# Kernel tuning notes

Measured on AMD Instinct MI355X. Metric: run time of the kernel, lower is better.

## Reference

```python
import jax, jax.numpy as jnp
import numpy as np

DIM = 4096
N_HEADS = 32
N_KV_HEADS = 8
HEAD_DIM = 128
SEQ = 2048
REPEATS = N_HEADS // N_KV_HEADS
SCALE = HEAD_DIM ** -0.5


def setup_inputs() -> dict:
    key = jax.random.key(0)
    ks = jax.random.split(key, 7)
    x = jax.random.normal(ks[0], (SEQ, DIM), dtype=jnp.float32)
    # rotary freqs_cis = exp(i * pos * theta^(-2j/d)) -> cos/sin, shape (S, head_dim/2)
    theta = 10000.0
    inv_freq = 1.0 / (theta ** (np.arange(0, HEAD_DIM, 2, dtype=np.float32) / HEAD_DIM))
    ang = np.arange(SEQ, dtype=np.float32)[:, None] * inv_freq[None, :]
    freqs_cos = jnp.asarray(np.cos(ang), dtype=jnp.float32)
    freqs_sin = jnp.asarray(np.sin(ang), dtype=jnp.float32)
    s = 0.02
    wq = s * jax.random.normal(ks[1], (DIM, N_HEADS * HEAD_DIM), dtype=jnp.float32)
    wk = s * jax.random.normal(ks[2], (DIM, N_KV_HEADS * HEAD_DIM), dtype=jnp.float32)
    wv = s * jax.random.normal(ks[3], (DIM, N_KV_HEADS * HEAD_DIM), dtype=jnp.float32)
    wo = s * jax.random.normal(ks[4], (N_HEADS * HEAD_DIM, DIM), dtype=jnp.float32)
    return {"x": x, "freqs_cos": freqs_cos, "freqs_sin": freqs_sin,
            "wq": wq, "wk": wk, "wv": wv, "wo": wo}


def _rope(t, cos, sin):
    # t: (S, H, D); treat last dim as D/2 complex pairs and rotate by freqs_cis
    S, H, D = t.shape
    tr = t.reshape(S, H, D // 2, 2)
    t1, t2 = tr[..., 0], tr[..., 1]
    c = cos[:, None, :]  # (S, 1, D/2)
    s = sin[:, None, :]
    o1 = t1 * c - t2 * s
    o2 = t1 * s + t2 * c
    return jnp.stack([o1, o2], axis=-1).reshape(S, H, D)


def reference(x, freqs_cos, freqs_sin, wq, wk, wv, wo):
    S = x.shape[0]
    xq = (x @ wq).reshape(S, N_HEADS, HEAD_DIM)
    xk = (x @ wk).reshape(S, N_KV_HEADS, HEAD_DIM)
    xv = (x @ wv).reshape(S, N_KV_HEADS, HEAD_DIM)
    xq = _rope(xq, freqs_cos, freqs_sin)
    xk = _rope(xk, freqs_cos, freqs_sin)
    # cache=None path: key,val = xk,xv; repeat_kv via repeat_interleave on head dim
    key = jnp.repeat(xk, REPEATS, axis=1)  # (S, H, D)
    val = jnp.repeat(xv, REPEATS, axis=1)
    # scaled dot-product attention, mask=None (cache is None)
    scores = jnp.einsum('qhd,khd->hqk', xq, key) * SCALE  # (H, S, S)
    att = jax.nn.softmax(scores, axis=-1)
    out = jnp.einsum('hqk,khd->qhd', att, val)  # (S, H, D)
    out = out.reshape(S, N_HEADS * HEAD_DIM)
    return out @ wo
```

## Files before the change

kernel.cpp:

```cpp
#include <hip/hip_runtime.h>
#include <hip/hip_bf16.h>

#define SEQ   2048
#define DIM   4096
#define NH    32
#define NKV   8
#define HD    128
#define KVDIM 1024
#define SCALE 0.08838834764831845f

typedef __attribute__((ext_vector_type(8))) short bf16x8;
typedef __attribute__((ext_vector_type(4))) float f32x4;
typedef __attribute__((ext_vector_type(16))) float f32x16;

__device__ __forceinline__ ushort f2bf(float f) {
  __hip_bfloat16 h = __float2bfloat16(f);
  return *reinterpret_cast<ushort*>(&h);
}

typedef const __attribute__((address_space(1))) uint* gas_ptr;
typedef __attribute__((address_space(3))) uint* las_ptr;
__device__ __forceinline__ void async16(const ushort* g, ushort* l) {
  __builtin_amdgcn_global_load_lds((gas_ptr)g, (las_ptr)l, 16, 0, 0);
}

__device__ __forceinline__ uint cvtpk(float lo, float hi) {
  uint r;
  asm("v_cvt_pk_bf16_f32 %0, %1, %2" : "=v"(r) : "v"(lo), "v"(hi));
  return r;
}
__device__ __forceinline__ void plswap(uint& a, uint& b) {
  asm("v_permlane32_swap_b32 %0, %1" : "+v"(a), "+v"(b));
}

__global__ __launch_bounds__(256) void convert_f32_bf16(
    const float* __restrict__ in, ushort* __restrict__ out)
{
  int i = (blockIdx.x * 256 + threadIdx.x) * 8;
  float4 a = *(const float4*)(in + i);
  float4 b = *(const float4*)(in + i + 4);
  uint4 u;
  u.x = (uint)f2bf(a.x) | ((uint)f2bf(a.y) << 16);
  u.y = (uint)f2bf(a.z) | ((uint)f2bf(a.w) << 16);
  u.z = (uint)f2bf(b.x) | ((uint)f2bf(b.y) << 16);
  u.w = (uint)f2bf(b.z) | ((uint)f2bf(b.w) << 16);
  *(uint4*)(out + i) = u;
}

__global__ __launch_bounds__(256) void transpose_w(
    const float* __restrict__ W, ushort* __restrict__ WT, int K, int N)
{
  __shared__ float t[32][33];
  const int k0 = blockIdx.y * 32, n0 = blockIdx.x * 32;
  const int tid = threadIdx.x;
  {
    int r = tid >> 3, c0 = (tid & 7) * 4;
    float4 v = *(const float4*)(W + (size_t)(k0 + r) * N + n0 + c0);
    t[r][c0] = v.x; t[r][c0 + 1] = v.y; t[r][c0 + 2] = v.z; t[r][c0 + 3] = v.w;
  }
  __syncthreads();
  {
    int n = tid >> 3, kc = (tid & 7) * 4;
    ushort4 u;
    u.x = f2bf(t[kc + 0][n]); u.y = f2bf(t[kc + 1][n]);
    u.z = f2bf(t[kc + 2][n]); u.w = f2bf(t[kc + 3][n]);
    *(ushort4*)(WT + (size_t)(n0 + n) * K + k0 + kc) = u;
  }
}

__global__ __launch_bounds__(256) void gemm_bt(
    const ushort* __restrict__ A, const ushort* __restrict__ BT,
    void* __restrict__ Cv, void* __restrict__ C2v,
    int M, int N, int K, int mode)
{
  __shared__ __align__(16) ushort As[128 * 32];
  __shared__ __align__(16) ushort Bs[128 * 32];

  const int tid  = threadIdx.x;
  const int lane = tid & 63;
  const int w    = tid >> 6;
  const int wr = w >> 1, wc = w & 1;
  const int quad = lane >> 4, l16 = lane & 15;
  const int m0 = blockIdx.y * 128, n0 = blockIdx.x * 128;
  const int srow = lane >> 2;
  const int scol = (lane & 3) * 8;

  f32x4 acc[4][4];
#pragma unroll
  for (int bm = 0; bm < 4; ++bm)
#pragma unroll
    for (int bn = 0; bn < 4; ++bn)
      acc[bm][bn] = (f32x4){0.f, 0.f, 0.f, 0.f};

  for (int k0 = 0; k0 < K; k0 += 32) {
#pragma unroll
    for (int j = 0; j < 2; ++j) {
      const int rb = w * 32 + j * 16;
      async16(A  + (size_t)(m0 + rb + srow) * K + k0 + scol, &As[rb * 32]);
      async16(BT + (size_t)(n0 + rb + srow) * K + k0 + scol, &Bs[rb * 32]);
    }
    __syncthreads();

    bf16x8 af[4], bf[4];
#pragma unroll
    for (int bm = 0; bm < 4; ++bm)
      af[bm] = *(const bf16x8*)&As[(wr * 64 + bm * 16 + l16) * 32 + quad * 8];
#pragma unroll
    for (int bn = 0; bn < 4; ++bn)
      bf[bn] = *(const bf16x8*)&Bs[(wc * 64 + bn * 16 + l16) * 32 + quad * 8];
#pragma unroll
    for (int bm = 0; bm < 4; ++bm)
#pragma unroll
      for (int bn = 0; bn < 4; ++bn)
        acc[bm][bn] = __builtin_amdgcn_mfma_f32_16x16x32_bf16(
            af[bm], bf[bn], acc[bm][bn], 0, 0, 0);
    __syncthreads();
  }

  if (mode == 0) {
    ushort* C = (ushort*)Cv;
#pragma unroll
    for (int bm = 0; bm < 4; ++bm) {
      int rbase = m0 + wr * 64 + bm * 16 + quad * 4;
#pragma unroll
      for (int bn = 0; bn < 4; ++bn) {
        int col = n0 + wc * 64 + bn * 16 + l16;
#pragma unroll
        for (int i = 0; i < 4; ++i)
          C[(size_t)(rbase + i) * N + col] = f2bf(acc[bm][bn][i]);
      }
    }
  } else if (mode == 1) {
    float* C = (float*)Cv;
#pragma unroll
    for (int bm = 0; bm < 4; ++bm) {
      int rbase = m0 + wr * 64 + bm * 16 + quad * 4;
#pragma unroll
      for (int bn = 0; bn < 4; ++bn) {
        int col = n0 + wc * 64 + bn * 16 + l16;
#pragma unroll
        for (int i = 0; i < 4; ++i)
          C[(size_t)(rbase + i) * N + col] = acc[bm][bn][i];
      }
    }
  } else {
    if (n0 < 1024) {
      ushort* C = (ushort*)Cv;
#pragma unroll
      for (int bm = 0; bm < 4; ++bm) {
        int rbase = m0 + wr * 64 + bm * 16 + quad * 4;
#pragma unroll
        for (int bn = 0; bn < 4; ++bn) {
          int col = n0 + wc * 64 + bn * 16 + l16;
#pragma unroll
          for (int i = 0; i < 4; ++i)
            C[(size_t)(rbase + i) * KVDIM + col] = f2bf(acc[bm][bn][i]);
        }
      }
    } else {
      ushort* C2 = (ushort*)C2v;
#pragma unroll
      for (int bm = 0; bm < 4; ++bm) {
        int rbase = m0 + wr * 64 + bm * 16 + quad * 4;
#pragma unroll
        for (int bn = 0; bn < 4; ++bn) {
          int col = n0 + wc * 64 + bn * 16 + l16 - 1024;
          ushort4 u;
          u.x = f2bf(acc[bm][bn][0]); u.y = f2bf(acc[bm][bn][1]);
          u.z = f2bf(acc[bm][bn][2]); u.w = f2bf(acc[bm][bn][3]);
          *(ushort4*)(C2 + (size_t)col * SEQ + rbase) = u;
        }
      }
    }
  }
}

__device__ __forceinline__ float bfhi(uint u) {
  union { uint i; float f; } v; v.i = u & 0xffff0000u; return v.f;
}
__device__ __forceinline__ float bflo(uint u) {
  union { uint i; float f; } v; v.i = u << 16; return v.f;
}
__global__ __launch_bounds__(256) void rope_kernel(
    ushort* __restrict__ t, const float* __restrict__ cosb,
    const float* __restrict__ sinb, int shift)
{
  int idx = blockIdx.x * 256 + threadIdx.x;
  int p  = idx & 63;
  int sh = idx >> 6;
  int s  = sh >> shift;
  uint* bp = (uint*)(t + ((size_t)sh << 7)) + p;
  uint u = *bp;
  float t1 = bflo(u), t2 = bfhi(u);
  float c  = cosb[(s << 6) + p];
  float sv = sinb[(s << 6) + p];
  float o1 = t1 * c - t2 * sv;
  float o2 = t1 * sv + t2 * c;
  *bp = ((uint)f2bf(o1)) | (((uint)f2bf(o2)) << 16);
}

#define OFF_V0U 8192
#define OFF_V1U 16384
#define NT (SEQ / 64)

__device__ __forceinline__ void stage_K(const ushort* __restrict__ K, ushort* SM,
                                        int w, int lane, int kb, int kvh) {
  const int r4 = lane >> 4, c16 = lane & 15;
#pragma unroll
  for (int j = 0; j < 4; ++j) {
    int rb = w * 16 + j * 4, row = rb + r4;
    int c = c16 ^ (row & 15);
    async16(K + (size_t)(kb + row) * KVDIM + kvh * HD + c * 8, &SM[rb * 128]);
  }
}
__device__ __forceinline__ void stage_V(const ushort* __restrict__ VT, ushort* SMv,
                                        int w, int lane, int kb, int kvh) {
  const int r8 = lane >> 3, c8 = lane & 7;
#pragma unroll
  for (int j = 0; j < 4; ++j) {
    int rb = w * 32 + j * 8, row = rb + r8;
    int c = c8 ^ (row & 7);
    async16(VT + (size_t)(kvh * 128 + row) * SEQ + kb + c * 8, &SMv[rb * 64]);
  }
}

__global__ __launch_bounds__(256, 2) void attn_mfma5(
    const ushort* __restrict__ Q, const ushort* __restrict__ K,
    const ushort* __restrict__ VT, ushort* __restrict__ O)
{
  __shared__ __align__(16) ushort SM[24576];

  const int tid = threadIdx.x, lane = tid & 63, w = tid >> 6;
  const int l31 = lane & 31, hi = lane >> 5;
  const int kx = l31 & 15;
  const int vx = lane & 7;
  const int h = blockIdx.y, kvh = h >> 2;
  const int q0 = blockIdx.x * 128;

  {
    const int r4 = lane >> 4, c16 = lane & 15;
#pragma unroll
    for (int j = 0; j < 8; ++j) {
      int rb = w * 32 + j * 4, row = rb + r4;
      int c = c16 ^ (row & 15);
      async16(Q + (size_t)(q0 + row) * DIM + h * HD + c * 8, &SM[rb * 128]);
    }
  }
  __syncthreads();

  bf16x8 qf[8];
#pragma unroll
  for (int ks = 0; ks < 8; ++ks) {
    int cc = ((2 * ks + hi) ^ kx) << 3;
    qf[ks] = *(const bf16x8*)&SM[(w * 32 + l31) * 128 + cc];
  }
  __syncthreads();

  stage_K(K, SM, w, lane, 0, kvh);
  stage_V(VT, &SM[OFF_V0U], w, lane, 0, kvh);

  f32x16 oacc[4];
#pragma unroll
  for (int dt = 0; dt < 4; ++dt)
#pragma unroll
    for (int r = 0; r < 16; ++r) oacc[dt][r] = 0.f;
  float m_i = -1e30f, l_i = 0.f;

  for (int t = 0; t < NT; ++t) {
    __syncthreads();

    f32x16 s0, s1;
#pragma unroll
    for (int r = 0; r < 16; ++r) { s0[r] = 0.f; s1[r] = 0.f; }
    __builtin_amdgcn_s_setprio(1);
#pragma unroll
    for (int ks = 0; ks < 8; ++ks) {
      int cc = ((2 * ks + hi) ^ kx) << 3;
      bf16x8 k0 = *(const bf16x8*)&SM[l31 * 128 + cc];
      bf16x8 k1 = *(const bf16x8*)&SM[(32 + l31) * 128 + cc];
      s0 = __builtin_amdgcn_mfma_f32_32x32x16_bf16(k0, qf[ks], s0, 0, 0, 0);
      s1 = __builtin_amdgcn_mfma_f32_32x32x16_bf16(k1, qf[ks], s1, 0, 0, 0);
    }
    __builtin_amdgcn_s_setprio(0);

    __syncthreads();

    if (t + 1 < NT) {
      stage_K(K, SM, w, lane, (t + 1) * 64, kvh);
      stage_V(VT, &SM[((t + 1) & 1) ? OFF_V1U : OFF_V0U], w, lane, (t + 1) * 64, kvh);
    }

    float tm[16];
#pragma unroll
    for (int i = 0; i < 16; ++i) tm[i] = fmaxf(s0[i], s1[i]);
#pragma unroll
    for (int d = 8; d >= 1; d >>= 1)
#pragma unroll
      for (int i = 0; i < 8; ++i) if (i < d) tm[i] = fmaxf(tm[i], tm[i + d]);
    float lm = fmaxf(tm[0], __shfl_xor(tm[0], 32));
    float lmS = lm * SCALE;
    float mn;
    if (__any(lmS > m_i + 8.0f)) {
      mn = fmaxf(m_i, lmS);
      float al = __expf(m_i - mn);
      m_i = mn; l_i *= al;
#pragma unroll
      for (int dt = 0; dt < 4; ++dt)
#pragma unroll
        for (int r = 0; r < 16; ++r) oacc[dt][r] *= al;
    } else mn = m_i;

    float p0[16], p1[16];
#pragma unroll
    for (int r = 0; r < 16; ++r) p0[r] = __expf(fmaf(s0[r], SCALE, -mn));
#pragma unroll
    for (int r = 0; r < 16; ++r) p1[r] = __expf(fmaf(s1[r], SCALE, -mn));
    {
      float ts[16];
#pragma unroll
      for (int i = 0; i < 16; ++i) ts[i] = p0[i] + p1[i];
#pragma unroll
      for (int d = 8; d >= 1; d >>= 1)
#pragma unroll
        for (int i = 0; i < 8; ++i) if (i < d) ts[i] += ts[i + d];
      l_i += ts[0] + __shfl_xor(ts[0], 32);
    }

    bf16x8 pf[4];
    {
      uint a0 = cvtpk(p0[0], p0[1]),  b0 = cvtpk(p0[4], p0[5]);   plswap(a0, b0);
      uint a1 = cvtpk(p0[2], p0[3]),  b1 = cvtpk(p0[6], p0[7]);   plswap(a1, b1);
      uint4 u0 = {a0, a1, b0, b1};  pf[0] = *(bf16x8*)&u0;
      uint a2 = cvtpk(p0[8], p0[9]),  b2 = cvtpk(p0[12], p0[13]); plswap(a2, b2);
      uint a3 = cvtpk(p0[10], p0[11]),b3 = cvtpk(p0[14], p0[15]); plswap(a3, b3);
      uint4 u1 = {a2, a3, b2, b3};  pf[1] = *(bf16x8*)&u1;
      uint a4 = cvtpk(p1[0], p1[1]),  b4 = cvtpk(p1[4], p1[5]);   plswap(a4, b4);
      uint a5 = cvtpk(p1[2], p1[3]),  b5 = cvtpk(p1[6], p1[7]);   plswap(a5, b5);
      uint4 u2 = {a4, a5, b4, b5};  pf[2] = *(bf16x8*)&u2;
      uint a6 = cvtpk(p1[8], p1[9]),  b6 = cvtpk(p1[12], p1[13]); plswap(a6, b6);
      uint a7 = cvtpk(p1[10], p1[11]),b7 = cvtpk(p1[14], p1[15]); plswap(a7, b7);
      uint4 u3 = {a6, a7, b6, b7};  pf[3] = *(bf16x8*)&u3;
    }

    const int vbU = (t & 1) ? OFF_V1U : OFF_V0U;
    __builtin_amdgcn_s_setprio(1);
#pragma unroll
    for (int ks = 0; ks < 4; ++ks) {
      int cc = ((2 * ks + hi) ^ vx) << 3;
#pragma unroll
      for (int dt = 0; dt < 4; ++dt) {
        bf16x8 vf = *(const bf16x8*)&SM[vbU + (dt * 32 + l31) * 64 + cc];
        oacc[dt] = __builtin_amdgcn_mfma_f32_32x32x16_bf16(vf, pf[ks], oacc[dt], 0, 0, 0);
      }
    }
    __builtin_amdgcn_s_setprio(0);
  }

  float linv = 1.0f / l_i;
  const int RB = w * 4096;
#pragma unroll
  for (int dt = 0; dt < 4; ++dt)
#pragma unroll
    for (int r = 0; r < 16; ++r) {
      int d = dt * 32 + (r & 3) + 8 * (r >> 2) + 4 * hi;
      SM[RB + l31 * 128 + (((d >> 3) ^ (l31 & 15)) << 3) + (d & 7)] =
          f2bf(oacc[dt][r] * linv);
    }
  {
    const int r4 = lane >> 4, c16 = lane & 15;
#pragma unroll
    for (int i = 0; i < 8; ++i) {
      int qq = i * 4 + r4;
      uint4 v = *(const uint4*)&SM[RB + qq * 128 + ((c16 ^ (qq & 15)) << 3)];
      *(uint4*)(O + (size_t)(q0 + w * 32 + qq) * DIM + h * HD + c16 * 8) = v;
    }
  }
}

extern "C" void kernel_launch(void* const* d_in, const int* in_sizes, int n_in,
                              void* d_out, int out_size, void* d_ws, size_t ws_size,
                              hipStream_t stream) {
  const float* x  = (const float*)d_in[0];
  const float* fc = (const float*)d_in[1];
  const float* fs = (const float*)d_in[2];
  const float* wq = (const float*)d_in[3];
  const float* wk = (const float*)d_in[4];
  const float* wv = (const float*)d_in[5];
  const float* wo = (const float*)d_in[6];
  float* out = (float*)d_out;

  ushort* xb   = (ushort*)d_ws;
  ushort* wT   = xb   + (size_t)SEQ * DIM;
  ushort* wkvT = wT   + (size_t)DIM * DIM;
  ushort* qb   = wkvT + (size_t)2048 * DIM;
  ushort* kb   = qb   + (size_t)SEQ * DIM;
  ushort* vT   = kb   + (size_t)SEQ * KVDIM;
  ushort* ab   = qb;

  dim3 blk(256);

  convert_f32_bf16<<<(SEQ * DIM) / 2048, blk, 0, stream>>>(x, xb);
  transpose_w<<<dim3(DIM / 32, DIM / 32), blk, 0, stream>>>(wq, wT, DIM, DIM);
  transpose_w<<<dim3(KVDIM / 32, DIM / 32), blk, 0, stream>>>(wk, wkvT, DIM, KVDIM);
  transpose_w<<<dim3(KVDIM / 32, DIM / 32), blk, 0, stream>>>(wv, wkvT + (size_t)KVDIM * DIM, DIM, KVDIM);

  gemm_bt<<<dim3(DIM / 128, SEQ / 128), blk, 0, stream>>>(xb, wT, qb, nullptr, SEQ, DIM, DIM, 0);
  gemm_bt<<<dim3(2048 / 128, SEQ / 128), blk, 0, stream>>>(xb, wkvT, kb, vT, SEQ, 2048, DIM, 2);

  rope_kernel<<<(SEQ * NH * 64) / 256, blk, 0, stream>>>(qb, fc, fs, 5);
  rope_kernel<<<(SEQ * NKV * 64) / 256, blk, 0, stream>>>(kb, fc, fs, 3);

  attn_mfma5<<<dim3(SEQ / 128, NH), blk, 0, stream>>>(qb, kb, vT, ab);

  transpose_w<<<dim3(DIM / 32, DIM / 32), blk, 0, stream>>>(wo, wT, DIM, DIM);
  gemm_bt<<<dim3(DIM / 128, SEQ / 128), blk, 0, stream>>>(ab, wT, out, nullptr, SEQ, DIM, DIM, 1);
}
```

Measured before the change: 603.1 us.

## Merge QKV projections into one GEMM and use swizzled 64-wide K tiles

The GEMM K-step doubles from 32 to 64, halving the number of barrier pairs per output tile. LDS tiles use an XOR swizzle so the MFMA fragment reads avoid bank conflicts. The separate Q and KV projection launches become a single 6144-wide GEMM launch over the contiguous wq/wkv transposed weights, with an epilogue that routes columns to Q, K or transposed V. The cost is twice the LDS per block, which may lower occupancy, plus more branching in the epilogue.

```diff
diff --git a/kernel.cpp b/kernel.cpp
--- a/kernel.cpp
+++ b/kernel.cpp
@@ -73,8 +73,8 @@
     void* __restrict__ Cv, void* __restrict__ C2v,
     int M, int N, int K, int mode)
 {
-  __shared__ __align__(16) ushort As[128 * 32];
-  __shared__ __align__(16) ushort Bs[128 * 32];
+  __shared__ __align__(16) ushort As[128 * 64];
+  __shared__ __align__(16) ushort Bs[128 * 64];
 
   const int tid  = threadIdx.x;
   const int lane = tid & 63;
@@ -82,8 +82,8 @@
   const int wr = w >> 1, wc = w & 1;
   const int quad = lane >> 4, l16 = lane & 15;
   const int m0 = blockIdx.y * 128, n0 = blockIdx.x * 128;
-  const int srow = lane >> 2;
-  const int scol = (lane & 3) * 8;
+  const int srow8 = lane >> 3;
+  const int sswz  = ((lane & 7) ^ srow8) << 3;
 
   f32x4 acc[4][4];
 #pragma unroll
@@ -92,28 +92,35 @@
     for (int bn = 0; bn < 4; ++bn)
       acc[bm][bn] = (f32x4){0.f, 0.f, 0.f, 0.f};
 
-  for (int k0 = 0; k0 < K; k0 += 32) {
-#pragma unroll
-    for (int j = 0; j < 2; ++j) {
-      const int rb = w * 32 + j * 16;
-      async16(A  + (size_t)(m0 + rb + srow) * K + k0 + scol, &As[rb * 32]);
-      async16(BT + (size_t)(n0 + rb + srow) * K + k0 + scol, &Bs[rb * 32]);
+  for (int k0 = 0; k0 < K; k0 += 64) {
+#pragma unroll
+    for (int j = 0; j < 4; ++j) {
+      const int rb = w * 32 + j * 8;
+      async16(A  + (size_t)(m0 + rb + srow8) * K + k0 + sswz, &As[rb * 64]);
+      async16(BT + (size_t)(n0 + rb + srow8) * K + k0 + sswz, &Bs[rb * 64]);
     }
     __syncthreads();
 
-    bf16x8 af[4], bf[4];
-#pragma unroll
-    for (int bm = 0; bm < 4; ++bm)
-      af[bm] = *(const bf16x8*)&As[(wr * 64 + bm * 16 + l16) * 32 + quad * 8];
-#pragma unroll
-    for (int bn = 0; bn < 4; ++bn)
-      bf[bn] = *(const bf16x8*)&Bs[(wc * 64 + bn * 16 + l16) * 32 + quad * 8];
-#pragma unroll
-    for (int bm = 0; bm < 4; ++bm)
-#pragma unroll
-      for (int bn = 0; bn < 4; ++bn)
-        acc[bm][bn] = __builtin_amdgcn_mfma_f32_16x16x32_bf16(
-            af[bm], bf[bn], acc[bm][bn], 0, 0, 0);
+#pragma unroll
+    for (int s = 0; s < 2; ++s) {
+      bf16x8 af[4], bf[4];
+#pragma unroll
+      for (int bm = 0; bm < 4; ++bm) {
+        const int row = wr * 64 + bm * 16 + l16;
+        af[bm] = *(const bf16x8*)&As[row * 64 + (((s * 4 + quad) ^ (row & 7)) << 3)];
+      }
+#pragma unroll
+      for (int bn = 0; bn < 4; ++bn) {
+        const int row = wc * 64 + bn * 16 + l16;
+        bf[bn] = *(const bf16x8*)&Bs[row * 64 + (((s * 4 + quad) ^ (row & 7)) << 3)];
+      }
+#pragma unroll
+      for (int bm = 0; bm < 4; ++bm)
+#pragma unroll
+        for (int bn = 0; bn < 4; ++bn)
+          acc[bm][bn] = __builtin_amdgcn_mfma_f32_16x16x32_bf16(
+              af[bm], bf[bn], acc[bm][bn], 0, 0, 0);
+    }
     __syncthreads();
   }
 
@@ -144,7 +151,7 @@
       }
     }
   } else {
-    if (n0 < 1024) {
+    if (n0 < 4096) {
       ushort* C = (ushort*)Cv;
 #pragma unroll
       for (int bm = 0; bm < 4; ++bm) {
@@ -152,19 +159,32 @@
 #pragma unroll
         for (int bn = 0; bn < 4; ++bn) {
           int col = n0 + wc * 64 + bn * 16 + l16;
+#pragma unroll
+          for (int i = 0; i < 4; ++i)
+            C[(size_t)(rbase + i) * DIM + col] = f2bf(acc[bm][bn][i]);
+        }
+      }
+    } else if (n0 < 5120) {
+      ushort* C = (ushort*)C2v;
+#pragma unroll
+      for (int bm = 0; bm < 4; ++bm) {
+        int rbase = m0 + wr * 64 + bm * 16 + quad * 4;
+#pragma unroll
+        for (int bn = 0; bn < 4; ++bn) {
+          int col = n0 + wc * 64 + bn * 16 + l16 - 4096;
 #pragma unroll
           for (int i = 0; i < 4; ++i)
             C[(size_t)(rbase + i) * KVDIM + col] = f2bf(acc[bm][bn][i]);
         }
       }
     } else {
-      ushort* C2 = (ushort*)C2v;
+      ushort* C2 = (ushort*)C2v + (size_t)SEQ * KVDIM;
 #pragma unroll
       for (int bm = 0; bm < 4; ++bm) {
         int rbase = m0 + wr * 64 + bm * 16 + quad * 4;
 #pragma unroll
         for (int bn = 0; bn < 4; ++bn) {
-          int col = n0 + wc * 64 + bn * 16 + l16 - 1024;
+          int col = n0 + wc * 64 + bn * 16 + l16 - 5120;
           ushort4 u;
           u.x = f2bf(acc[bm][bn][0]); u.y = f2bf(acc[bm][bn][1]);
           u.z = f2bf(acc[bm][bn][2]); u.w = f2bf(acc[bm][bn][3]);
@@ -404,8 +424,7 @@
   transpose_w<<<dim3(KVDIM / 32, DIM / 32), blk, 0, stream>>>(wk, wkvT, DIM, KVDIM);
   transpose_w<<<dim3(KVDIM / 32, DIM / 32), blk, 0, stream>>>(wv, wkvT + (size_t)KVDIM * DIM, DIM, KVDIM);
 
-  gemm_bt<<<dim3(DIM / 128, SEQ / 128), blk, 0, stream>>>(xb, wT, qb, nullptr, SEQ, DIM, DIM, 0);
-  gemm_bt<<<dim3(2048 / 128, SEQ / 128), blk, 0, stream>>>(xb, wkvT, kb, vT, SEQ, 2048, DIM, 2);
+  gemm_bt<<<dim3(6144 / 128, SEQ / 128), blk, 0, stream>>>(xb, wT, qb, kb, SEQ, 6144, DIM, 2);
 
   rope_kernel<<<(SEQ * NH * 64) / 256, blk, 0, stream>>>(qb, fc, fs, 5);
   rope_kernel<<<(SEQ * NKV * 64) / 256, blk, 0, stream>>>(kb, fc, fs, 3);
```

New measurement: 540.5 us. -10.4%, faster.
